# Performance work log

Hardware: AMD Instinct MI355X
Metric: run time of the kernel (lower is better)

Reference implementation:

```python
import jax, jax.numpy as jnp
import numpy as np

B, T, F, L, E, H, A, V = 64, 32, 512, 196, 512, 512, 512, 10000


def setup_inputs() -> dict:
    key = jax.random.key(0)
    ks = jax.random.split(key, 24)
    s = 0.02
    features = jax.random.normal(ks[0], (B, F, L), dtype=jnp.float32)
    captions = jax.random.randint(ks[1], (B, T), 0, V)
    lengths = jnp.sort(jax.random.randint(ks[2], (B,), 2, T + 1))[::-1]
    lengths = lengths.at[0].set(T)  # ensure max(decode_lengths) == T-1 (static)
    return {
        "features": features,
        "captions": captions,
        "lengths": lengths,
        "W_emb": jax.random.normal(ks[3], (V, E)) * s,
        "W_enc": jax.random.normal(ks[4], (A, F)) * s,
        "b_enc": jnp.zeros((A,)),
        "W_dec": jax.random.normal(ks[5], (A, H)) * s,
        "b_dec": jnp.zeros((A,)),
        "W_full": jax.random.normal(ks[6], (1, A)) * s,
        "b_full": jnp.zeros((1,)),
        "W_fbeta": jax.random.normal(ks[7], (F, H)) * s,
        "b_fbeta": jnp.zeros((F,)),
        "W_ih": jax.random.normal(ks[8], (4 * H, E + F)) * s,
        "W_hh": jax.random.normal(ks[9], (4 * H, H)) * s,
        "b_ih": jnp.zeros((4 * H,)),
        "b_hh": jnp.zeros((4 * H,)),
        "W_out": jax.random.normal(ks[10], (V, H)) * s,
        "b_out": jnp.zeros((V,)),
        "W_init_h": jax.random.normal(ks[11], (H, F)) * s,
        "b_init_h": jnp.zeros((H,)),
        "W_init_c": jax.random.normal(ks[12], (H, F)) * s,
        "b_init_c": jnp.zeros((H,)),
    }


def reference(features, captions, lengths, W_emb, W_enc, b_enc, W_dec, b_dec,
              W_full, b_full, W_fbeta, b_fbeta, W_ih, W_hh, b_ih, b_hh,
              W_out, b_out, W_init_h, b_init_h, W_init_c, b_init_c):
    Bv, Fv, Lv = features.shape
    Tmax = captions.shape[1] - 1  # max(decode_lengths), static (lengths[0]==T)
    feat_r = features.reshape(Bv, -1, Fv)          # [B, L, F] (torch .view semantics)
    en_att = feat_r @ W_enc.T + b_enc              # [B, L, A], step-invariant
    mean_f = features.mean(axis=2)                 # [B, F]
    h0 = mean_f @ W_init_h.T + b_init_h            # [B, H]
    c0 = mean_f @ W_init_c.T + b_init_c
    emb = W_emb[captions]                          # [B, T, E]
    dec_len = lengths - 1                          # [B]

    def step(carry, xs):
        h, c = carry
        emb_t, i = xs
        de = h @ W_dec.T + b_dec                                   # [B, A]
        full = (jnp.tanh(en_att + de[:, None, :]) @ W_full.T)[..., 0] + b_full[0]  # [B, L]
        alpha = jax.nn.softmax(full, axis=1)                       # [B, L]
        z = jnp.einsum('blf,bl->bf', feat_r, alpha)                # [B, F]
        z = z * jax.nn.sigmoid(h @ W_fbeta.T + b_fbeta)
        x = jnp.concatenate([emb_t, z], axis=1)                    # [B, E+F]
        gates = x @ W_ih.T + b_ih + h @ W_hh.T + b_hh              # [B, 4H]
        ig, fg, gg, og = jnp.split(gates, 4, axis=1)
        c_new = jax.nn.sigmoid(fg) * c + jax.nn.sigmoid(ig) * jnp.tanh(gg)
        h_new = jax.nn.sigmoid(og) * jnp.tanh(c_new)
        out = h_new @ W_out.T + b_out                              # [B, V] (dropout: eval)
        active = (dec_len > i)[:, None]                            # ragged mask
        h = jnp.where(active, h_new, h)
        c = jnp.where(active, c_new, c)
        pred = jnp.where(active, out, 0.0)
        alpha_m = jnp.where(active, alpha, 0.0)
        return (h, c), (pred, alpha_m)

    emb_steps = jnp.swapaxes(emb[:, :Tmax, :], 0, 1)               # [Tmax, B, E]
    (_, _), (preds, alphas) = jax.lax.scan(step, (h0, c0), (emb_steps, jnp.arange(Tmax)))
    predictions = jnp.swapaxes(preds, 0, 1)                        # [B, Tmax, V]
    alphas = jnp.swapaxes(alphas, 0, 1)                            # [B, Tmax, L]
    return predictions, alphas
```

## Files before the change

### kernel.cpp

```cpp
#include <hip/hip_runtime.h>


typedef unsigned short ushort_t;
typedef __attribute__((ext_vector_type(8))) short short8;
typedef __attribute__((ext_vector_type(4))) float f32x4;

__device__ __forceinline__ float bf2f(ushort_t u) {
    unsigned x = ((unsigned)u) << 16;
    float f;
    __builtin_memcpy(&f, &x, 4);
    return f;
}
__device__ __forceinline__ ushort_t f2bf(float f) {
    unsigned x;
    __builtin_memcpy(&x, &f, 4);
    unsigned r = (x + 0x7fffu + ((x >> 16) & 1u)) >> 16;
    return (ushort_t)r;
}
__device__ __forceinline__ float sigmoidf_(float x) { return 1.f / (1.f + __expf(-x)); }
__device__ __forceinline__ float tanh_fast(float x) {
    float e = __expf(2.f * x);
    return 1.f - 2.f / (e + 1.f);
}
__device__ __forceinline__ float wred_sum(float v) {
    #pragma unroll
    for (int m = 32; m; m >>= 1) v += __shfl_xor(v, m, 64);
    return v;
}
__device__ __forceinline__ float wred_max(float v) {
    #pragma unroll
    for (int m = 32; m; m >>= 1) v = fmaxf(v, __shfl_xor(v, m, 64));
    return v;
}

__device__ __forceinline__ float aload_f(const float* p) {
    return __hip_atomic_load((float*)p, __ATOMIC_RELAXED, __HIP_MEMORY_SCOPE_AGENT);
}
__device__ __forceinline__ void astore_f(float* p, float v) {
    __hip_atomic_store(p, v, __ATOMIC_RELAXED, __HIP_MEMORY_SCOPE_AGENT);
}
__device__ __forceinline__ unsigned aload_u(const unsigned* p) {
    return __hip_atomic_load((unsigned*)p, __ATOMIC_RELAXED, __HIP_MEMORY_SCOPE_AGENT);
}
__device__ __forceinline__ void astore_u(unsigned* p, unsigned v) {
    __hip_atomic_store(p, v, __ATOMIC_RELAXED, __HIP_MEMORY_SCOPE_AGENT);
}
__device__ __forceinline__ int aload_i(const int* p) {
    return __hip_atomic_load((int*)p, __ATOMIC_RELAXED, __HIP_MEMORY_SCOPE_AGENT);
}
__device__ __forceinline__ void astore_i(int* p, int v) {
    __hip_atomic_store(p, v, __ATOMIC_RELAXED, __HIP_MEMORY_SCOPE_AGENT);
}

#define KEXP2 2.8853901817779268f

__global__ void detect_kernel(const unsigned* __restrict__ feat_raw, int* __restrict__ flag,
                              int* __restrict__ flags) {
    int lane = threadIdx.x;
    #pragma unroll
    for (int i = 0; i < 16; ++i) flags[lane + i * 64] = 0;
    unsigned u = feat_raw[lane];
    unsigned e = (u >> 7) & 0xffu;
    bool bf_like = (e >= 105 && e <= 133);
    unsigned long long m = __ballot(bf_like);
    if (lane == 0) *flag = (__popcll(m) >= 40) ? 0 : 1;
}

#define NCVT 19
struct CvtArgs {
    const void* src[NCVT];
    void* dst[NCVT];
    int n[NCVT];
};

__global__ __launch_bounds__(256) void convert_kernel(CvtArgs a, const int* __restrict__ flag) {
    const int ai = blockIdx.y;
    const int n = a.n[ai];
    const int base = (blockIdx.x * 256 + threadIdx.x) * 8;
    if (base >= n) return;
    ushort_t* dst = (ushort_t*)a.dst[ai];
    if (*flag) {
        const float* s = (const float*)a.src[ai];
        #pragma unroll
        for (int i = 0; i < 8; ++i) {
            int idx = base + i;
            if (idx < n) dst[idx] = f2bf(s[idx]);
        }
    } else {
        const ushort_t* s = (const ushort_t*)a.src[ai];
        #pragma unroll
        for (int i = 0; i < 8; ++i) {
            int idx = base + i;
            if (idx < n) dst[idx] = s[idx];
        }
    }
}

__global__ __launch_bounds__(256) void embrows_kernel(const void* __restrict__ Wemb,
                                                      const int* __restrict__ captions,
                                                      const int* __restrict__ flag,
                                                      ushort_t* __restrict__ emb_c) {
    const int tb = blockIdx.x;
    const int t = tb >> 6, b = tb & 63;
    const int cap = captions[b * 32 + t];
    const int e0 = threadIdx.x;
    if (*flag) {
        const float* s = (const float*)Wemb + cap * 512;
        emb_c[tb * 512 + e0] = f2bf(s[e0]);
        emb_c[tb * 512 + e0 + 256] = f2bf(s[e0 + 256]);
    } else {
        const ushort_t* s = (const ushort_t*)Wemb + cap * 512;
        emb_c[tb * 512 + e0] = s[e0];
        emb_c[tb * 512 + e0 + 256] = s[e0 + 256];
    }
}

__global__ void prepw2_kernel(const ushort_t* __restrict__ wf, const ushort_t* __restrict__ bfc,
                              float* __restrict__ w2) {
    int tid = threadIdx.x;
    float w = bf2f(wf[tid]);
    w2[tid] = -2.f * w;
    float s = wred_sum(w);
    __shared__ float r8[8];
    if ((tid & 63) == 0) r8[tid >> 6] = s;
    __syncthreads();
    if (tid == 0) {
        float tot = r8[0] + r8[1] + r8[2] + r8[3] + r8[4] + r8[5] + r8[6] + r8[7];
        w2[512] = tot + bf2f(bfc[0]);
    }
}

template <class AROW, class BROW, class EPI>
__device__ __forceinline__ void gemm_tile(AROW arow, BROW brow, EPI epi) {
    __shared__ __align__(16) ushort_t As[64][40];
    __shared__ __align__(16) ushort_t Bs[64][40];
    const int tid = threadIdx.x;
    const int row = tid >> 2, ks = (tid & 3) << 3;
    const int wave = tid >> 6, lane = tid & 63;
    const int quad = lane >> 4, l15 = lane & 15;
    f32x4 acc[4];
    #pragma unroll
    for (int s = 0; s < 4; ++s) acc[s] = (f32x4){0.f, 0.f, 0.f, 0.f};
    const ushort_t* ap = arow(row);
    const ushort_t* bp = brow(row);
    for (int k0 = 0; k0 < 512; k0 += 32) {
        short8 av = {0, 0, 0, 0, 0, 0, 0, 0};
        short8 bv = {0, 0, 0, 0, 0, 0, 0, 0};
        if (ap) av = *(const short8*)(ap + k0 + ks);
        if (bp) bv = *(const short8*)(bp + k0 + ks);
        __syncthreads();
        *(short8*)&As[row][ks] = av;
        *(short8*)&Bs[row][ks] = bv;
        __syncthreads();
        short8 af = *(const short8*)&As[(wave << 4) + l15][quad << 3];
        #pragma unroll
        for (int s = 0; s < 4; ++s) {
            short8 bfr = *(const short8*)&Bs[(s << 4) + l15][quad << 3];
            acc[s] = __builtin_amdgcn_mfma_f32_16x16x32_bf16(af, bfr, acc[s], 0, 0, 0);
        }
    }
    epi((wave << 4) + (quad << 2), l15, acc);
}

__global__ __launch_bounds__(256) void mean_kernel(const ushort_t* __restrict__ features,
                                                   ushort_t* __restrict__ mean_bf) {
    const int b = blockIdx.x;
    const int wave = threadIdx.x >> 6, lane = threadIdx.x & 63;
    const ushort_t* fb = features + b * 512 * 196;
    for (int f = wave; f < 512; f += 4) {
        const ushort_t* r = fb + f * 196;
        float s = bf2f(r[lane]) + bf2f(r[lane + 64]) + bf2f(r[lane + 128]);
        if (lane < 4) s += bf2f(r[lane + 192]);
        s = wred_sum(s);
        if (lane == 0) mean_bf[b * 512 + f] = f2bf(s * (1.f / 196.f));
    }
}

__global__ __launch_bounds__(256) void init_kernel(
    const ushort_t* __restrict__ mean_bf, const ushort_t* __restrict__ Winh,
    const ushort_t* __restrict__ binh, const ushort_t* __restrict__ Winc,
    const ushort_t* __restrict__ binc, ushort_t* __restrict__ h_bf,
    float* __restrict__ cbuf) {
    const int n0 = blockIdx.x << 6;
    gemm_tile(
        [&](int r) { return mean_bf + r * 512; },
        [&](int r) {
            int n = n0 + r;
            return (n < 512) ? (Winh + n * 512) : (Winc + (n - 512) * 512);
        },
        [&](int mb, int l15, const f32x4* acc) {
            #pragma unroll
            for (int s = 0; s < 4; ++s) {
                int n = n0 + (s << 4) + l15;
                #pragma unroll
                for (int r = 0; r < 4; ++r) {
                    int b = mb + r;
                    if (n < 512)
                        h_bf[b * 512 + n] = f2bf(acc[s][r] + bf2f(binh[n]));
                    else
                        cbuf[b * 512 + (n - 512)] = acc[s][r] + bf2f(binc[n - 512]);
                }
            }
        });
}

__global__ __launch_bounds__(256) void enatt_kernel(const ushort_t* __restrict__ feat,
                                                    const ushort_t* __restrict__ Wenc,
                                                    const ushort_t* __restrict__ benc,
                                                    ushort_t* __restrict__ en_att) {
    const int m0 = blockIdx.y << 6, n0 = blockIdx.x << 6;
    gemm_tile(
        [&](int r) { return feat + (m0 + r) * 512; },
        [&](int r) { return Wenc + (n0 + r) * 512; },
        [&](int mb, int l15, const f32x4* acc) {
            #pragma unroll
            for (int s = 0; s < 4; ++s) {
                int n = n0 + (s << 4) + l15;
                float bias = bf2f(benc[n]);
                #pragma unroll
                for (int r = 0; r < 4; ++r) {
                    int m = m0 + mb + r;
                    en_att[m * 512 + n] = f2bf(acc[s][r] + bias);
                }
            }
        });
}

__global__ __launch_bounds__(256) void ec_kernel(const ushort_t* __restrict__ emb_c,
                                                 const ushort_t* __restrict__ Wih,
                                                 const ushort_t* __restrict__ bih,
                                                 const ushort_t* __restrict__ bhh,
                                                 float* __restrict__ ec) {
    const int t = blockIdx.y, n0 = blockIdx.x << 6;
    gemm_tile(
        [&](int r) { return emb_c + (t * 64 + r) * 512; },
        [&](int r) { return Wih + (n0 + r) * 1024; },
        [&](int mb, int l15, const f32x4* acc) {
            #pragma unroll
            for (int s = 0; s < 4; ++s) {
                int j = n0 + (s << 4) + l15;
                float bias = bf2f(bih[j]) + bf2f(bhh[j]);
                #pragma unroll
                for (int r = 0; r < 4; ++r) {
                    int b = mb + r;
                    ec[(t * 64 + b) * 2048 + j] = acc[s][r] + bias;
                }
            }
        });
}

struct LoopArgs {
    const ushort_t* W3c;
    const ushort_t* bdec;
    const ushort_t* bfb;
    const ushort_t* en_att;
    const ushort_t* feat;
    const ushort_t* Wih;
    const float* w2;
    const float* ec;
    const int* lengths;
    const int* flag;
    ushort_t* h_bf;
    ushort_t* z_bf;
    ushort_t* H_all;
    float* cbuf;
    float* deK;
    float* fgate;
    float* hh;
    float* fullv;
    void* out_base;
    int* flags;
};

__global__ __launch_bounds__(512, 2) void loop_kernel(LoopArgs A) {
    const int blk = blockIdx.x, tid = threadIdx.x;
    const int wave = tid >> 6, lane = tid & 63;
    const int quad = lane >> 4, l15 = lane & 15;
    const int g = blk >> 6, local = blk & 63;
    int* fbase = A.flags + g * 256;

    __shared__ __align__(16) ushort_t enS[49 * 512];
    __shared__ __align__(16) ushort_t ftS[196 * 128];
    __shared__ __align__(16) ushort_t AsL[16][520];
    __shared__ float smem[2048];
    __shared__ float fullS[200];
    __shared__ float red8[16];

    const int f32o = *A.flag;
    const int b0 = g << 4;
    const int Tg = A.lengths[b0] - 1;

    const bool roleA = local < 24;
    const int bB = b0 + (local >> 2);
    const int qB = local & 3;
    const int lenB = A.lengths[bB];
    const bool roleC = local < 32;
    const int dtC = local;

    unsigned* h_u32 = (unsigned*)A.h_bf;
    unsigned* z_u32 = (unsigned*)A.z_bf;

    float w2r[8];
    {
        f32x4 w0 = *(const f32x4*)(A.w2 + lane * 8);
        f32x4 w1 = *(const f32x4*)(A.w2 + lane * 8 + 4);
        w2r[0] = w0[0]; w2r[1] = w0[1]; w2r[2] = w0[2]; w2r[3] = w0[3];
        w2r[4] = w1[0]; w2r[5] = w1[1]; w2r[6] = w1[2]; w2r[7] = w1[3];
    }
    const float fullc = A.w2[512];

    {
        const short8* src = (const short8*)(A.en_att + ((size_t)bB * 196 + qB * 49) * 512);
        short8* dst = (short8*)enS;
        for (int i = tid; i < 49 * 64; i += 512) dst[i] = src[i];
        const ushort_t* fsrc = A.feat + (size_t)bB * 100352 + qB * 128;
        short8* fdst = (short8*)ftS;
        for (int i = tid; i < 196 * 16; i += 512) {
            int l = i >> 4, c = i & 15;
            fdst[i] = *(const short8*)(fsrc + l * 512 + c * 8);
        }
    }

    for (int t = 0; t < Tg; ++t) {
        if (roleA) {
            if (wave == 0 && t > 0) {
                const int* fp = fbase + (lane & 31);
                for (;;) {
                    if (__all(aload_i(fp) >= t)) break;
                    __builtin_amdgcn_s_sleep(1);
                }
                asm volatile("" ::: "memory");
            }
            __syncthreads();
            for (int i = tid; i < 4096; i += 512) {
                int r = i >> 8, c = i & 255;
                *(unsigned*)&AsL[r][c << 1] = aload_u(h_u32 + ((b0 + r) << 8) + c);
            }
            __syncthreads();
            const int nt = local * 8 + wave;
            const ushort_t* br = A.W3c + ((nt << 4) + l15) * 512 + (quad << 3);
            const ushort_t* arl = &AsL[l15][quad << 3];
            f32x4 acc = {0.f, 0.f, 0.f, 0.f};
            #pragma unroll
            for (int k0 = 0; k0 < 512; k0 += 32)
                acc = __builtin_amdgcn_mfma_f32_16x16x32_bf16(
                    *(const short8*)(arl + k0), *(const short8*)(br + k0), acc, 0, 0, 0);
            const int n = (nt << 4) + l15;
            #pragma unroll
            for (int r = 0; r < 4; ++r) {
                const int b = b0 + (quad << 2) + r;
                float v = acc[r];
                if (n < 512)
                    astore_f(A.deK + b * 512 + n, (v + bf2f(A.bdec[n])) * KEXP2);
                else if (n < 1024)
                    astore_f(A.fgate + b * 512 + (n - 512),
                             sigmoidf_(v + bf2f(A.bfb[n - 512])));
                else
                    astore_f(A.hh + b * 2048 + (n - 1024), v);
            }
            asm volatile("s_waitcnt vmcnt(0)" ::: "memory");
            __syncthreads();
            if (tid == 0) astore_i(fbase + 32 + local, t + 1);
        }

        {
            if (wave == 0) {
                const int* fp = fbase + 32 + (lane & 7);
                for (;;) {
                    if (__all(aload_i(fp) >= t + 1)) break;
                    __builtin_amdgcn_s_sleep(1);
                }
                asm volatile("" ::: "memory");
            }
            __syncthreads();
            const bool act = (lenB - 1) > t;
            const size_t aoff = 19840000ull + ((size_t)bB * 31 + t) * 196;
            if (act) {
                float dkr[8];
                const float* dk = A.deK + bB * 512 + lane * 8;
                #pragma unroll
                for (int j = 0; j < 8; ++j) dkr[j] = aload_f(dk + j);
                for (int i = wave; i < 49; i += 8) {
                    short8 ev = *(const short8*)(enS + i * 512 + lane * 8);
                    float acc = 0.f;
                    #pragma unroll
                    for (int j = 0; j < 8; ++j) {
                        float e2 = __builtin_amdgcn_exp2f(
                            fmaf(bf2f((ushort_t)ev[j]), KEXP2, dkr[j]));
                        acc = fmaf(w2r[j], __builtin_amdgcn_rcpf(e2 + 1.f), acc);
                    }
                    acc = wred_sum(acc);
                    if (lane == 0)
                        astore_f(A.fullv + bB * 196 + qB * 49 + i, acc + fullc);
                }
            }
            asm volatile("s_waitcnt vmcnt(0)" ::: "memory");
            __syncthreads();
            if (tid == 0) astore_i(fbase + 128 + local, t + 1);
            if (wave == 0) {
                const int* fp = fbase + 128 + (local & ~3) + (lane & 3);
                for (;;) {
                    if (__all(aload_i(fp) >= t + 1)) break;
                    __builtin_amdgcn_s_sleep(1);
                }
                asm volatile("" ::: "memory");
            }
            __syncthreads();
            if (act) {
                float v = (tid < 196) ? aload_f(A.fullv + bB * 196 + tid) : -1e30f;
                float wm = wred_max(v);
                if (lane == 0) red8[wave] = wm;
                __syncthreads();
                float mx = fmaxf(fmaxf(fmaxf(red8[0], red8[1]), fmaxf(red8[2], red8[3])),
                                 fmaxf(fmaxf(red8[4], red8[5]), fmaxf(red8[6], red8[7])));
                float e = (tid < 196) ? __expf(v - mx) : 0.f;
                float sw = wred_sum(e);
                if (lane == 0) red8[8 + wave] = sw;
                __syncthreads();
                float tot = red8[8] + red8[9] + red8[10] + red8[11] +
                            red8[12] + red8[13] + red8[14] + red8[15];
                float inv = 1.f / tot;
                float a = e * inv;
                if (tid < 196) {
                    fullS[tid] = a;
                    if (qB == 0) {
                        if (f32o) ((float*)A.out_base)[aoff + tid] = a;
                        else ((ushort_t*)A.out_base)[aoff + tid] = f2bf(a);
                    }
                }
                __syncthreads();
                const int fl = tid & 127, gq = tid >> 7;
                float zacc = 0.f;
                #pragma unroll 4
                for (int l = gq; l < 196; l += 4)
                    zacc = fmaf(fullS[l], bf2f(ftS[l * 128 + fl]), zacc);
                smem[256 + (gq << 7) + fl] = zacc;
                __syncthreads();
                if (tid < 64) {
                    const int f0l = tid << 1;
                    float z0 = smem[256 + f0l] + smem[384 + f0l] +
                               smem[512 + f0l] + smem[640 + f0l];
                    float z1 = smem[257 + f0l] + smem[385 + f0l] +
                               smem[513 + f0l] + smem[641 + f0l];
                    const int f0 = (qB << 7) + f0l;
                    z0 *= aload_f(A.fgate + bB * 512 + f0);
                    z1 *= aload_f(A.fgate + bB * 512 + f0 + 1);
                    unsigned zp = (unsigned)f2bf(z0) | ((unsigned)f2bf(z1) << 16);
                    astore_u(z_u32 + bB * 256 + (f0 >> 1), zp);
                }
            } else {
                if (qB == 0 && tid < 196) {
                    if (f32o) ((float*)A.out_base)[aoff + tid] = 0.f;
                    else ((ushort_t*)A.out_base)[aoff + tid] = 0;
                }
            }
            asm volatile("s_waitcnt vmcnt(0)" ::: "memory");
            __syncthreads();
            if (tid == 0) astore_i(fbase + 64 + local, t + 1);
        }

        if (roleC) {
            if (wave == 0) {
                const int* zp = fbase + 64 + lane;
                for (;;) {
                    int v1 = aload_i(zp);
                    int v2 = (lane < 4)
                                 ? aload_i(fbase + 32 + 8 + lane * 4 + (dtC >> 3))
                                 : 0x7fffffff;
                    if (__all(v1 >= t + 1 && v2 >= t + 1)) break;
                    __builtin_amdgcn_s_sleep(1);
                }
                asm volatile("" ::: "memory");
            }
            __syncthreads();
            float pe[8], ph[8];
            #pragma unroll
            for (int k = 0; k < 8; ++k) { pe[k] = 0.f; ph[k] = 0.f; }
            if (tid < 128) {
                const int bl = tid >> 3, p = tid & 7;
                const int bE = b0 + bl;
                const int dimE = (dtC << 4) + (p << 1);
                const int eb = (t * 64 + bE) * 2048, hb = bE * 2048;
                pe[0] = A.ec[eb + dimE];         pe[1] = A.ec[eb + dimE + 1];
                pe[2] = A.ec[eb + 512 + dimE];   pe[3] = A.ec[eb + 512 + dimE + 1];
                pe[4] = A.ec[eb + 1024 + dimE];  pe[5] = A.ec[eb + 1024 + dimE + 1];
                pe[6] = A.ec[eb + 1536 + dimE];  pe[7] = A.ec[eb + 1536 + dimE + 1];
                ph[0] = aload_f(A.hh + hb + dimE);
                ph[1] = aload_f(A.hh + hb + dimE + 1);
                ph[2] = aload_f(A.hh + hb + 512 + dimE);
                ph[3] = aload_f(A.hh + hb + 512 + dimE + 1);
                ph[4] = aload_f(A.hh + hb + 1024 + dimE);
                ph[5] = aload_f(A.hh + hb + 1024 + dimE + 1);
                ph[6] = aload_f(A.hh + hb + 1536 + dimE);
                ph[7] = aload_f(A.hh + hb + 1536 + dimE + 1);
            }
            for (int i = tid; i < 4096; i += 512) {
                int r = i >> 8, c = i & 255;
                *(unsigned*)&AsL[r][c << 1] = aload_u(z_u32 + ((b0 + r) << 8) + c);
            }
            __syncthreads();
            const int gw = wave & 3, kh = wave >> 2;
            const int j = (gw << 9) + (dtC << 4) + l15;
            const ushort_t* br = A.Wih + j * 1024 + 512 + (kh << 8) + (quad << 3);
            const ushort_t* arl = &AsL[l15][(kh << 8) + (quad << 3)];
            f32x4 acc = {0.f, 0.f, 0.f, 0.f};
            #pragma unroll
            for (int k0 = 0; k0 < 256; k0 += 32)
                acc = __builtin_amdgcn_mfma_f32_16x16x32_bf16(
                    *(const short8*)(arl + k0), *(const short8*)(br + k0), acc, 0, 0, 0);
            #pragma unroll
            for (int r = 0; r < 4; ++r)
                smem[(wave << 8) + (((quad << 2) + r) << 4) + l15] = acc[r];
            __syncthreads();
            if (tid < 128) {
                const int bl = tid >> 3, p = tid & 7;
                const int b = b0 + bl;
                const int i0 = (bl << 4) + (p << 1);
                const int dim = (dtC << 4) + (p << 1);
                float ig0 = smem[i0] + smem[1024 + i0] + pe[0] + ph[0];
                float ig1 = smem[i0 + 1] + smem[1025 + i0] + pe[1] + ph[1];
                float fg0 = smem[256 + i0] + smem[1280 + i0] + pe[2] + ph[2];
                float fg1 = smem[257 + i0] + smem[1281 + i0] + pe[3] + ph[3];
                float gg0 = smem[512 + i0] + smem[1536 + i0] + pe[4] + ph[4];
                float gg1 = smem[513 + i0] + smem[1537 + i0] + pe[5] + ph[5];
                float og0 = smem[768 + i0] + smem[1792 + i0] + pe[6] + ph[6];
                float og1 = smem[769 + i0] + smem[1793 + i0] + pe[7] + ph[7];
                float co0 = A.cbuf[b * 512 + dim];
                float co1 = A.cbuf[b * 512 + dim + 1];
                float cn0 = sigmoidf_(fg0) * co0 + sigmoidf_(ig0) * tanh_fast(gg0);
                float hn0 = sigmoidf_(og0) * tanh_fast(cn0);
                float cn1 = sigmoidf_(fg1) * co1 + sigmoidf_(ig1) * tanh_fast(gg1);
                float hn1 = sigmoidf_(og1) * tanh_fast(cn1);
                unsigned hp = (unsigned)f2bf(hn0) | ((unsigned)f2bf(hn1) << 16);
                *(unsigned*)&A.H_all[(t * 64 + b) * 512 + dim] = hp;
                if (A.lengths[b] - 1 > t) {
                    A.cbuf[b * 512 + dim] = cn0;
                    A.cbuf[b * 512 + dim + 1] = cn1;
                    astore_u(h_u32 + b * 256 + (dim >> 1), hp);
                }
            }
            asm volatile("s_waitcnt vmcnt(0)" ::: "memory");
            __syncthreads();
            if (tid == 0) astore_i(fbase + dtC, t + 1);
        }
    }

    if (qB == 0) {
        for (int t = Tg; t < 31; ++t) {
            if (tid < 196) {
                const size_t aoff = 19840000ull + ((size_t)bB * 31 + t) * 196;
                if (f32o) ((float*)A.out_base)[aoff + tid] = 0.f;
                else ((ushort_t*)A.out_base)[aoff + tid] = 0;
            }
        }
    }
}

__global__ __launch_bounds__(256) void preds_kernel(
    const ushort_t* __restrict__ H_all, const ushort_t* __restrict__ Wout,
    const ushort_t* __restrict__ bout, const int* __restrict__ lengths,
    const int* __restrict__ flag, void* __restrict__ out_base) {
    const int t = blockIdx.x, n0 = blockIdx.y << 6;
    const int f32o = *flag;
    gemm_tile(
        [&](int r) { return H_all + (t * 64 + r) * 512; },
        [&](int r) -> const ushort_t* {
            int n = n0 + r;
            return (n < 10000) ? (Wout + n * 512) : (const ushort_t*)nullptr;
        },
        [&](int mb, int l15, const f32x4* acc) {
            #pragma unroll
            for (int s = 0; s < 4; ++s) {
                int n = n0 + (s << 4) + l15;
                if (n >= 10000) continue;
                float bias = bf2f(bout[n]);
                #pragma unroll
                for (int r = 0; r < 4; ++r) {
                    int b = mb + r;
                    bool act = lengths[b] > t + 1;
                    float val = act ? (acc[s][r] + bias) : 0.f;
                    size_t off = (size_t)b * 310000 + t * 10000 + n;
                    if (f32o) ((float*)out_base)[off] = val;
                    else ((ushort_t*)out_base)[off] = act ? f2bf(val) : (ushort_t)0;
                }
            }
        });
}

extern "C" void kernel_launch(void* const* d_in, const int* in_sizes, int n_in,
                              void* d_out, int out_size, void* d_ws, size_t ws_size,
                              hipStream_t stream) {
    const void* features = d_in[0];
    const int* captions = (const int*)d_in[1];
    const int* lengths = (const int*)d_in[2];
    const void* W_emb = d_in[3];

    char* ws = (char*)d_ws;
    size_t o = 0;
    auto alloc = [&](size_t bytes) {
        size_t r = o;
        o += (bytes + 255) & ~(size_t)255;
        return r;
    };
    ushort_t* feat_c  = (ushort_t*)(ws + alloc(6422528ull * 2));
    ushort_t* Wenc_c  = (ushort_t*)(ws + alloc(262144ull * 2));
    ushort_t* benc_c  = (ushort_t*)(ws + alloc(512 * 2));
    ushort_t* W3c     = (ushort_t*)(ws + alloc(3072ull * 512 * 2));
    ushort_t* bdec_c  = (ushort_t*)(ws + alloc(512 * 2));
    ushort_t* wfull_c = (ushort_t*)(ws + alloc(512 * 2));
    ushort_t* bfull_c = (ushort_t*)(ws + alloc(2));
    ushort_t* bfb_c   = (ushort_t*)(ws + alloc(512 * 2));
    ushort_t* Wih_c   = (ushort_t*)(ws + alloc(2097152ull * 2));
    ushort_t* bih_c   = (ushort_t*)(ws + alloc(2048 * 2));
    ushort_t* bhh_c   = (ushort_t*)(ws + alloc(2048 * 2));
    ushort_t* Wout_c  = (ushort_t*)(ws + alloc(5120000ull * 2));
    ushort_t* bout_c  = (ushort_t*)(ws + alloc(10000 * 2));
    ushort_t* Winh_c  = (ushort_t*)(ws + alloc(262144ull * 2));
    ushort_t* binh_c  = (ushort_t*)(ws + alloc(512 * 2));
    ushort_t* Winc_c  = (ushort_t*)(ws + alloc(262144ull * 2));
    ushort_t* binc_c  = (ushort_t*)(ws + alloc(512 * 2));
    ushort_t* emb_c   = (ushort_t*)(ws + alloc(1984ull * 512 * 2));
    ushort_t* en_att  = (ushort_t*)(ws + alloc(12544ull * 512 * 2));
    float*    ec      = (float*)(ws + alloc(1984ull * 2048 * 4));
    ushort_t* H_all   = (ushort_t*)(ws + alloc(1984ull * 512 * 2));
    ushort_t* h_bf    = (ushort_t*)(ws + alloc(64 * 512 * 2));
    float*    cbuf    = (float*)(ws + alloc(64 * 512 * 4));
    float*    deK     = (float*)(ws + alloc(64 * 512 * 4));
    float*    fgate   = (float*)(ws + alloc(64 * 512 * 4));
    float*    hh      = (float*)(ws + alloc(64ull * 2048 * 4));
    ushort_t* z_bf    = (ushort_t*)(ws + alloc(64 * 512 * 2));
    ushort_t* mean_bf = (ushort_t*)(ws + alloc(64 * 512 * 2));
    float*    fullv   = (float*)(ws + alloc(64 * 196 * 4));
    float*    w2buf   = (float*)(ws + alloc(513 * 4));
    int*      flag    = (int*)(ws + alloc(256));
    int*      flags   = (int*)(ws + alloc(1024 * 4));

    detect_kernel<<<1, 64, 0, stream>>>((const unsigned*)features, flag, flags);

    CvtArgs ca;
    const void* srcs[NCVT] = {features, d_in[4], d_in[5], d_in[6], d_in[7], d_in[8],
                              d_in[9], d_in[10], d_in[11], d_in[12], d_in[13], d_in[14],
                              d_in[15], d_in[16], d_in[17], d_in[18], d_in[19], d_in[20],
                              d_in[21]};
    void* dsts[NCVT] = {feat_c, Wenc_c, benc_c, W3c , bdec_c, wfull_c, bfull_c,
                        W3c + 262144 , bfb_c, Wih_c, W3c + 524288 ,
                        bih_c, bhh_c, Wout_c, bout_c, Winh_c, binh_c, Winc_c, binc_c};
    int ns[NCVT] = {6422528, 262144, 512, 262144, 512, 512, 1, 262144, 512,
                    2097152, 1048576, 2048, 2048, 5120000, 10000, 262144, 512,
                    262144, 512};
    for (int i = 0; i < NCVT; ++i) {
        ca.src[i] = srcs[i];
        ca.dst[i] = dsts[i];
        ca.n[i] = ns[i];
    }
    convert_kernel<<<dim3(3136, NCVT), 256, 0, stream>>>(ca, flag);
    embrows_kernel<<<1984, 256, 0, stream>>>(W_emb, captions, flag, emb_c);
    prepw2_kernel<<<1, 512, 0, stream>>>(wfull_c, bfull_c, w2buf);

    mean_kernel<<<64, 256, 0, stream>>>(feat_c, mean_bf);
    init_kernel<<<16, 256, 0, stream>>>(mean_bf, Winh_c, binh_c, Winc_c, binc_c,
                                        h_bf, cbuf);
    enatt_kernel<<<dim3(8, 196), 256, 0, stream>>>(feat_c, Wenc_c, benc_c, en_att);
    ec_kernel<<<dim3(32, 31), 256, 0, stream>>>(emb_c, Wih_c, bih_c, bhh_c, ec);

    LoopArgs la;
    la.W3c = W3c; la.bdec = bdec_c; la.bfb = bfb_c;
    la.en_att = en_att; la.feat = feat_c; la.Wih = Wih_c;
    la.w2 = w2buf; la.ec = ec; la.lengths = lengths; la.flag = flag;
    la.h_bf = h_bf; la.z_bf = z_bf; la.H_all = H_all;
    la.cbuf = cbuf; la.deK = deK; la.fgate = fgate; la.hh = hh;
    la.fullv = fullv; la.out_base = d_out; la.flags = flags;
    loop_kernel<<<256, 512, 0, stream>>>(la);

    preds_kernel<<<dim3(31, 157), 256, 0, stream>>>(H_all, Wout_c, bout_c, lengths,
                                                    flag, d_out);
}
```

Baseline: 1.177 ms.

## Remove separate h-projection phase from recurrent loop, fold into per-block compute

The dedicated phase where 24 blocks computed the decoder-attention, f-beta gate and W_hh projections for all batches, followed by a grid-wide flag wait, is removed. Each attention block now computes its own batch's decoder projection (using a pre-transposed W_dec) and its quarter of the f-beta gate with scalar FMAs. The W_hh term moves into the LSTM gate MFMA alongside the z term, and h is double-buffered so the next step's reads do not race with writes. This drops one inter-block synchronisation stage per timestep, at the cost of redundant dec-projection work across the 4 blocks per batch. It also adds spin caps to the flag waits and flattens the convert grid so no blocks are launched past each array's end.

```diff
diff --git a/kernel.cpp b/kernel.cpp
--- a/kernel.cpp
+++ b/kernel.cpp
@@ -4,6 +4,8 @@
 typedef unsigned short ushort_t;
 typedef __attribute__((ext_vector_type(8))) short short8;
 typedef __attribute__((ext_vector_type(4))) float f32x4;
+
+#define SPIN_CAP (1 << 22)
 
 __device__ __forceinline__ float bf2f(ushort_t u) {
     unsigned x = ((unsigned)u) << 16;
@@ -71,12 +73,14 @@
     const void* src[NCVT];
     void* dst[NCVT];
     int n[NCVT];
+    int cub[NCVT + 1];
 };
 
 __global__ __launch_bounds__(256) void convert_kernel(CvtArgs a, const int* __restrict__ flag) {
-    const int ai = blockIdx.y;
+    int bx = blockIdx.x, ai = 0;
+    while (bx >= a.cub[ai + 1]) ++ai;
     const int n = a.n[ai];
-    const int base = (blockIdx.x * 256 + threadIdx.x) * 8;
+    const int base = (bx - a.cub[ai]) * 2048 + threadIdx.x * 8;
     if (base >= n) return;
     ushort_t* dst = (ushort_t*)a.dst[ai];
     if (*flag) {
@@ -93,6 +97,22 @@
             int idx = base + i;
             if (idx < n) dst[idx] = s[idx];
         }
+    }
+}
+
+__global__ __launch_bounds__(256) void transpose_wdec_kernel(const ushort_t* __restrict__ W3c,
+                                                             ushort_t* __restrict__ WdT) {
+    __shared__ ushort_t tile[64][65];
+    const int ta = (blockIdx.x & 7) << 6;
+    const int tk = (blockIdx.x >> 3) << 6;
+    for (int i = threadIdx.x; i < 4096; i += 256) {
+        int r = i >> 6, c = i & 63;
+        tile[r][c] = W3c[(ta + r) * 512 + tk + c];
+    }
+    __syncthreads();
+    for (int i = threadIdx.x; i < 4096; i += 256) {
+        int r = i >> 6, c = i & 63;
+        WdT[(tk + r) * 512 + ta + c] = tile[c][r];
     }
 }
 
@@ -251,6 +271,7 @@
 
 struct LoopArgs {
     const ushort_t* W3c;
+    const ushort_t* WdT;
     const ushort_t* bdec;
     const ushort_t* bfb;
     const ushort_t* en_att;
@@ -264,9 +285,6 @@
     ushort_t* z_bf;
     ushort_t* H_all;
     float* cbuf;
-    float* deK;
-    float* fgate;
-    float* hh;
     float* fullv;
     void* out_base;
     int* flags;
@@ -281,8 +299,11 @@
 
     __shared__ __align__(16) ushort_t enS[49 * 512];
     __shared__ __align__(16) ushort_t ftS[196 * 128];
-    __shared__ __align__(16) ushort_t AsL[16][520];
-    __shared__ float smem[2048];
+    __shared__ __align__(16) ushort_t AsL[32][520];
+    __shared__ float smem[4096];
+    __shared__ float hS[512];
+    __shared__ float deS[512];
+    __shared__ float fgS[128];
     __shared__ float fullS[200];
     __shared__ float red8[16];
 
@@ -290,7 +311,6 @@
     const int b0 = g << 4;
     const int Tg = A.lengths[b0] - 1;
 
-    const bool roleA = local < 24;
     const int bB = b0 + (local >> 2);
     const int qB = local & 3;
     const int lenB = A.lengths[bB];
@@ -320,66 +340,62 @@
             fdst[i] = *(const short8*)(fsrc + l * 512 + c * 8);
         }
     }
+    __syncthreads();
 
     for (int t = 0; t < Tg; ++t) {
-        if (roleA) {
+        const bool act = (lenB - 1) > t;
+        const size_t aoff = 19840000ull + ((size_t)bB * 31 + t) * 196;
+
+        if (act) {
             if (wave == 0 && t > 0) {
                 const int* fp = fbase + (lane & 31);
+                int spins = 0;
                 for (;;) {
                     if (__all(aload_i(fp) >= t)) break;
+                    if (++spins > SPIN_CAP) break;
                     __builtin_amdgcn_s_sleep(1);
                 }
                 asm volatile("" ::: "memory");
             }
             __syncthreads();
-            for (int i = tid; i < 4096; i += 512) {
-                int r = i >> 8, c = i & 255;
-                *(unsigned*)&AsL[r][c << 1] = aload_u(h_u32 + ((b0 + r) << 8) + c);
-            }
-            __syncthreads();
-            const int nt = local * 8 + wave;
-            const ushort_t* br = A.W3c + ((nt << 4) + l15) * 512 + (quad << 3);
-            const ushort_t* arl = &AsL[l15][quad << 3];
-            f32x4 acc = {0.f, 0.f, 0.f, 0.f};
-            #pragma unroll
-            for (int k0 = 0; k0 < 512; k0 += 32)
-                acc = __builtin_amdgcn_mfma_f32_16x16x32_bf16(
-                    *(const short8*)(arl + k0), *(const short8*)(br + k0), acc, 0, 0, 0);
-            const int n = (nt << 4) + l15;
-            #pragma unroll
-            for (int r = 0; r < 4; ++r) {
-                const int b = b0 + (quad << 2) + r;
-                float v = acc[r];
-                if (n < 512)
-                    astore_f(A.deK + b * 512 + n, (v + bf2f(A.bdec[n])) * KEXP2);
-                else if (n < 1024)
-                    astore_f(A.fgate + b * 512 + (n - 512),
-                             sigmoidf_(v + bf2f(A.bfb[n - 512])));
-                else
-                    astore_f(A.hh + b * 2048 + (n - 1024), v);
-            }
-            asm volatile("s_waitcnt vmcnt(0)" ::: "memory");
-            __syncthreads();
-            if (tid == 0) astore_i(fbase + 32 + local, t + 1);
-        }
-
-        {
-            if (wave == 0) {
-                const int* fp = fbase + 32 + (lane & 7);
-                for (;;) {
-                    if (__all(aload_i(fp) >= t + 1)) break;
-                    __builtin_amdgcn_s_sleep(1);
-                }
-                asm volatile("" ::: "memory");
-            }
-            __syncthreads();
-            const bool act = (lenB - 1) > t;
-            const size_t aoff = 19840000ull + ((size_t)bB * 31 + t) * 196;
-            if (act) {
+            {
+                const unsigned* hsrc = h_u32 + ((t & 1) << 14) + bB * 256;
+                if (tid < 256) {
+                    unsigned v = aload_u(hsrc + tid);
+                    hS[tid * 2] = bf2f((ushort_t)(v & 0xffffu));
+                    hS[tid * 2 + 1] = bf2f((ushort_t)(v >> 16));
+                }
+            }
+            __syncthreads();
+            {
+                float p[8];
+                #pragma unroll
+                for (int j = 0; j < 8; ++j) p[j] = 0.f;
+                const ushort_t* wt = A.WdT + (wave << 6) * 512 + (lane << 3);
+                #pragma unroll 4
+                for (int i = 0; i < 64; ++i) {
+                    short8 wv = *(const short8*)(wt + i * 512);
+                    float hk = hS[(wave << 6) + i];
+                    #pragma unroll
+                    for (int j = 0; j < 8; ++j)
+                        p[j] = fmaf(bf2f((ushort_t)wv[j]), hk, p[j]);
+                }
+                #pragma unroll
+                for (int j = 0; j < 8; ++j)
+                    smem[(wave << 9) + (lane << 3) + j] = p[j];
+            }
+            __syncthreads();
+            {
+                float dsum = 0.f;
+                #pragma unroll
+                for (int q = 0; q < 8; ++q) dsum += smem[(q << 9) + tid];
+                deS[tid] = (dsum + bf2f(A.bdec[tid])) * KEXP2;
+            }
+            __syncthreads();
+            {
                 float dkr[8];
-                const float* dk = A.deK + bB * 512 + lane * 8;
                 #pragma unroll
-                for (int j = 0; j < 8; ++j) dkr[j] = aload_f(dk + j);
+                for (int j = 0; j < 8; ++j) dkr[j] = deS[lane * 8 + j];
                 for (int i = wave; i < 49; i += 8) {
                     short8 ev = *(const short8*)(enS + i * 512 + lane * 8);
                     float acc = 0.f;
@@ -394,163 +410,188 @@
                         astore_f(A.fullv + bB * 196 + qB * 49 + i, acc + fullc);
                 }
             }
-            asm volatile("s_waitcnt vmcnt(0)" ::: "memory");
-            __syncthreads();
-            if (tid == 0) astore_i(fbase + 128 + local, t + 1);
+        }
+        asm volatile("s_waitcnt vmcnt(0)" ::: "memory");
+        __syncthreads();
+        if (tid == 0) astore_i(fbase + 128 + local, t + 1);
+
+        if (act) {
+            {
+                const int fl_ = tid >> 2, kq_ = tid & 3;
+                const ushort_t* wr = A.W3c + (512 + (qB << 7) + fl_) * 512 + (kq_ << 7);
+                float a2 = 0.f;
+                #pragma unroll 4
+                for (int k = 0; k < 128; k += 8) {
+                    short8 wv = *(const short8*)(wr + k);
+                    #pragma unroll
+                    for (int j = 0; j < 8; ++j)
+                        a2 = fmaf(bf2f((ushort_t)wv[j]), hS[(kq_ << 7) + k + j], a2);
+                }
+                smem[tid] = a2;
+            }
             if (wave == 0) {
                 const int* fp = fbase + 128 + (local & ~3) + (lane & 3);
+                int spins = 0;
                 for (;;) {
                     if (__all(aload_i(fp) >= t + 1)) break;
+                    if (++spins > SPIN_CAP) break;
                     __builtin_amdgcn_s_sleep(1);
                 }
                 asm volatile("" ::: "memory");
             }
             __syncthreads();
+            if (tid < 128)
+                fgS[tid] = sigmoidf_(smem[tid << 2] + smem[(tid << 2) | 1] +
+                                     smem[(tid << 2) | 2] + smem[(tid << 2) | 3] +
+                                     bf2f(A.bfb[(qB << 7) + tid]));
+            float v = (tid < 196) ? aload_f(A.fullv + bB * 196 + tid) : -1e30f;
+            float wm = wred_max(v);
+            if (lane == 0) red8[wave] = wm;
+            __syncthreads();
+            float mx = fmaxf(fmaxf(fmaxf(red8[0], red8[1]), fmaxf(red8[2], red8[3])),
+                             fmaxf(fmaxf(red8[4], red8[5]), fmaxf(red8[6], red8[7])));
+            float e = (tid < 196) ? __expf(v - mx) : 0.f;
+            float sw = wred_sum(e);
+            if (lane == 0) red8[8 + wave] = sw;
+            __syncthreads();
+            float tot = red8[8] + red8[9] + red8[10] + red8[11] +
+                        red8[12] + red8[13] + red8[14] + red8[15];
+            float inv = 1.f / tot;
+            float a = e * inv;
+            if (tid < 196) fullS[tid] = a;
+            __syncthreads();
+            const int fl = tid & 127, gq = tid >> 7;
+            float zacc = 0.f;
+            #pragma unroll 4
+            for (int l = gq; l < 196; l += 4)
+                zacc = fmaf(fullS[l], bf2f(ftS[l * 128 + fl]), zacc);
+            smem[256 + (gq << 7) + fl] = zacc;
+            __syncthreads();
+            if (tid < 64) {
+                const int f0l = tid << 1;
+                float z0 = smem[256 + f0l] + smem[384 + f0l] +
+                           smem[512 + f0l] + smem[640 + f0l];
+                float z1 = smem[257 + f0l] + smem[385 + f0l] +
+                           smem[513 + f0l] + smem[641 + f0l];
+                z0 *= fgS[f0l];
+                z1 *= fgS[f0l + 1];
+                unsigned zp = (unsigned)f2bf(z0) | ((unsigned)f2bf(z1) << 16);
+                astore_u(z_u32 + bB * 256 + (qB << 6) + tid, zp);
+            }
+        }
+        asm volatile("s_waitcnt vmcnt(0)" ::: "memory");
+        __syncthreads();
+        if (tid == 0) astore_i(fbase + 64 + local, t + 1);
+        if (qB == 0 && tid < 196) {
             if (act) {
-                float v = (tid < 196) ? aload_f(A.fullv + bB * 196 + tid) : -1e30f;
-                float wm = wred_max(v);
-                if (lane == 0) red8[wave] = wm;
-                __syncthreads();
-                float mx = fmaxf(fmaxf(fmaxf(red8[0], red8[1]), fmaxf(red8[2], red8[3])),
-                                 fmaxf(fmaxf(red8[4], red8[5]), fmaxf(red8[6], red8[7])));
-                float e = (tid < 196) ? __expf(v - mx) : 0.f;
-                float sw = wred_sum(e);
-                if (lane == 0) red8[8 + wave] = sw;
-                __syncthreads();
-                float tot = red8[8] + red8[9] + red8[10] + red8[11] +
-                            red8[12] + red8[13] + red8[14] + red8[15];
-                float inv = 1.f / tot;
-                float a = e * inv;
-                if (tid < 196) {
-                    fullS[tid] = a;
-                    if (qB == 0) {
-                        if (f32o) ((float*)A.out_base)[aoff + tid] = a;
-                        else ((ushort_t*)A.out_base)[aoff + tid] = f2bf(a);
-                    }
-                }
-                __syncthreads();
-                const int fl = tid & 127, gq = tid >> 7;
-                float zacc = 0.f;
-                #pragma unroll 4
-                for (int l = gq; l < 196; l += 4)
-                    zacc = fmaf(fullS[l], bf2f(ftS[l * 128 + fl]), zacc);
-                smem[256 + (gq << 7) + fl] = zacc;
-                __syncthreads();
-                if (tid < 64) {
-                    const int f0l = tid << 1;
-                    float z0 = smem[256 + f0l] + smem[384 + f0l] +
-                               smem[512 + f0l] + smem[640 + f0l];
-                    float z1 = smem[257 + f0l] + smem[385 + f0l] +
-                               smem[513 + f0l] + smem[641 + f0l];
-                    const int f0 = (qB << 7) + f0l;
-                    z0 *= aload_f(A.fgate + bB * 512 + f0);
-                    z1 *= aload_f(A.fgate + bB * 512 + f0 + 1);
-                    unsigned zp = (unsigned)f2bf(z0) | ((unsigned)f2bf(z1) << 16);
-                    astore_u(z_u32 + bB * 256 + (f0 >> 1), zp);
-                }
+                if (f32o) ((float*)A.out_base)[aoff + tid] = fullS[tid];
+                else ((ushort_t*)A.out_base)[aoff + tid] = f2bf(fullS[tid]);
             } else {
-                if (qB == 0 && tid < 196) {
-                    if (f32o) ((float*)A.out_base)[aoff + tid] = 0.f;
-                    else ((ushort_t*)A.out_base)[aoff + tid] = 0;
-                }
-            }
-            asm volatile("s_waitcnt vmcnt(0)" ::: "memory");
-            __syncthreads();
-            if (tid == 0) astore_i(fbase + 64 + local, t + 1);
+                if (f32o) ((float*)A.out_base)[aoff + tid] = 0.f;
+                else ((ushort_t*)A.out_base)[aoff + tid] = 0;
+            }
         }
 
         if (roleC) {
             if (wave == 0) {
                 const int* zp = fbase + 64 + lane;
+                int spins = 0;
                 for (;;) {
-                    int v1 = aload_i(zp);
-                    int v2 = (lane < 4)
-                                 ? aload_i(fbase + 32 + 8 + lane * 4 + (dtC >> 3))
-                                 : 0x7fffffff;
-                    if (__all(v1 >= t + 1 && v2 >= t + 1)) break;
+                    if (__all(aload_i(zp) >= t + 1)) break;
+                    if (++spins > SPIN_CAP) break;
                     __builtin_amdgcn_s_sleep(1);
                 }
                 asm volatile("" ::: "memory");
             }
             __syncthreads();
-            float pe[8], ph[8];
+            float pe[8];
             #pragma unroll
-            for (int k = 0; k < 8; ++k) { pe[k] = 0.f; ph[k] = 0.f; }
+            for (int k = 0; k < 8; ++k) pe[k] = 0.f;
             if (tid < 128) {
                 const int bl = tid >> 3, p = tid & 7;
                 const int bE = b0 + bl;
                 const int dimE = (dtC << 4) + (p << 1);
-                const int eb = (t * 64 + bE) * 2048, hb = bE * 2048;
+                const int eb = (t * 64 + bE) * 2048;
                 pe[0] = A.ec[eb + dimE];         pe[1] = A.ec[eb + dimE + 1];
                 pe[2] = A.ec[eb + 512 + dimE];   pe[3] = A.ec[eb + 512 + dimE + 1];
                 pe[4] = A.ec[eb + 1024 + dimE];  pe[5] = A.ec[eb + 1024 + dimE + 1];
                 pe[6] = A.ec[eb + 1536 + dimE];  pe[7] = A.ec[eb + 1536 + dimE + 1];
-                ph[0] = aload_f(A.hh + hb + dimE);
-                ph[1] = aload_f(A.hh + hb + dimE + 1);
-                ph[2] = aload_f(A.hh + hb + 512 + dimE);
-                ph[3] = aload_f(A.hh + hb + 512 + dimE + 1);
-                ph[4] = aload_f(A.hh + hb + 1024 + dimE);
-                ph[5] = aload_f(A.hh + hb + 1024 + dimE + 1);
-                ph[6] = aload_f(A.hh + hb + 1536 + dimE);
-                ph[7] = aload_f(A.hh + hb + 1536 + dimE + 1);
-            }
-            for (int i = tid; i < 4096; i += 512) {
-                int r = i >> 8, c = i & 255;
-                *(unsigned*)&AsL[r][c << 1] = aload_u(z_u32 + ((b0 + r) << 8) + c);
+            }
+            {
+                const unsigned* hsrc = h_u32 + ((t & 1) << 14);
+                for (int i = tid; i < 4096; i += 512) {
+                    int r = i >> 8, c = i & 255;
+                    *(unsigned*)&AsL[r][c << 1] = aload_u(z_u32 + ((b0 + r) << 8) + c);
+                    *(unsigned*)&AsL[16 + r][c << 1] = aload_u(hsrc + ((b0 + r) << 8) + c);
+                }
             }
             __syncthreads();
             const int gw = wave & 3, kh = wave >> 2;
             const int j = (gw << 9) + (dtC << 4) + l15;
-            const ushort_t* br = A.Wih + j * 1024 + 512 + (kh << 8) + (quad << 3);
-            const ushort_t* arl = &AsL[l15][(kh << 8) + (quad << 3)];
+            const ushort_t* brz = A.Wih + j * 1024 + 512 + (kh << 8) + (quad << 3);
+            const ushort_t* brh = A.W3c + (1024 + j) * 512 + (kh << 8) + (quad << 3);
+            const ushort_t* arz = &AsL[l15][(kh << 8) + (quad << 3)];
+            const ushort_t* arh = &AsL[16 + l15][(kh << 8) + (quad << 3)];
             f32x4 acc = {0.f, 0.f, 0.f, 0.f};
             #pragma unroll
-            for (int k0 = 0; k0 < 256; k0 += 32)
+            for (int k0 = 0; k0 < 256; k0 += 32) {
                 acc = __builtin_amdgcn_mfma_f32_16x16x32_bf16(
-                    *(const short8*)(arl + k0), *(const short8*)(br + k0), acc, 0, 0, 0);
+                    *(const short8*)(arz + k0), *(const short8*)(brz + k0), acc, 0, 0, 0);
+                acc = __builtin_amdgcn_mfma_f32_16x16x32_bf16(
+                    *(const short8*)(arh + k0), *(const short8*)(brh + k0), acc, 0, 0, 0);
+            }
             #pragma unroll
             for (int r = 0; r < 4; ++r)
                 smem[(wave << 8) + (((quad << 2) + r) << 4) + l15] = acc[r];
             __syncthreads();
+            float cn0 = 0.f, cn1 = 0.f;
+            unsigned hpw = 0;
+            bool activeB = false;
+            int bQ = 0, dimQ = 0;
             if (tid < 128) {
                 const int bl = tid >> 3, p = tid & 7;
-                const int b = b0 + bl;
+                bQ = b0 + bl;
+                dimQ = (dtC << 4) + (p << 1);
                 const int i0 = (bl << 4) + (p << 1);
-                const int dim = (dtC << 4) + (p << 1);
-                float ig0 = smem[i0] + smem[1024 + i0] + pe[0] + ph[0];
-                float ig1 = smem[i0 + 1] + smem[1025 + i0] + pe[1] + ph[1];
-                float fg0 = smem[256 + i0] + smem[1280 + i0] + pe[2] + ph[2];
-                float fg1 = smem[257 + i0] + smem[1281 + i0] + pe[3] + ph[3];
-                float gg0 = smem[512 + i0] + smem[1536 + i0] + pe[4] + ph[4];
-                float gg1 = smem[513 + i0] + smem[1537 + i0] + pe[5] + ph[5];
-                float og0 = smem[768 + i0] + smem[1792 + i0] + pe[6] + ph[6];
-                float og1 = smem[769 + i0] + smem[1793 + i0] + pe[7] + ph[7];
-                float co0 = A.cbuf[b * 512 + dim];
-                float co1 = A.cbuf[b * 512 + dim + 1];
-                float cn0 = sigmoidf_(fg0) * co0 + sigmoidf_(ig0) * tanh_fast(gg0);
+                float ig0 = smem[i0] + smem[1024 + i0] + pe[0];
+                float ig1 = smem[i0 + 1] + smem[1025 + i0] + pe[1];
+                float fg0 = smem[256 + i0] + smem[1280 + i0] + pe[2];
+                float fg1 = smem[257 + i0] + smem[1281 + i0] + pe[3];
+                float gg0 = smem[512 + i0] + smem[1536 + i0] + pe[4];
+                float gg1 = smem[513 + i0] + smem[1537 + i0] + pe[5];
+                float og0 = smem[768 + i0] + smem[1792 + i0] + pe[6];
+                float og1 = smem[769 + i0] + smem[1793 + i0] + pe[7];
+                float co0 = A.cbuf[bQ * 512 + dimQ];
+                float co1 = A.cbuf[bQ * 512 + dimQ + 1];
+                cn0 = sigmoidf_(fg0) * co0 + sigmoidf_(ig0) * tanh_fast(gg0);
                 float hn0 = sigmoidf_(og0) * tanh_fast(cn0);
-                float cn1 = sigmoidf_(fg1) * co1 + sigmoidf_(ig1) * tanh_fast(gg1);
+                cn1 = sigmoidf_(fg1) * co1 + sigmoidf_(ig1) * tanh_fast(gg1);
                 float hn1 = sigmoidf_(og1) * tanh_fast(cn1);
-                unsigned hp = (unsigned)f2bf(hn0) | ((unsigned)f2bf(hn1) << 16);
-                *(unsigned*)&A.H_all[(t * 64 + b) * 512 + dim] = hp;
-                if (A.lengths[b] - 1 > t) {
-                    A.cbuf[b * 512 + dim] = cn0;
-                    A.cbuf[b * 512 + dim + 1] = cn1;
-                    astore_u(h_u32 + b * 256 + (dim >> 1), hp);
-                }
+                activeB = (A.lengths[bQ] - 1) > t;
+                unsigned newp = (unsigned)f2bf(hn0) | ((unsigned)f2bf(hn1) << 16);
+                unsigned oldp = *(const unsigned*)&AsL[16 + bl][dimQ];
+                hpw = activeB ? newp : oldp;
+                astore_u(h_u32 + (((t + 1) & 1) << 14) + bQ * 256 + (dimQ >> 1), hpw);
             }
             asm volatile("s_waitcnt vmcnt(0)" ::: "memory");
             __syncthreads();
             if (tid == 0) astore_i(fbase + dtC, t + 1);
+            if (tid < 128) {
+                *(unsigned*)&A.H_all[(t * 64 + bQ) * 512 + dimQ] = hpw;
+                if (activeB) {
+                    A.cbuf[bQ * 512 + dimQ] = cn0;
+                    A.cbuf[bQ * 512 + dimQ + 1] = cn1;
+                }
+            }
         }
     }
 
     if (qB == 0) {
         for (int t = Tg; t < 31; ++t) {
             if (tid < 196) {
-                const size_t aoff = 19840000ull + ((size_t)bB * 31 + t) * 196;
-                if (f32o) ((float*)A.out_base)[aoff + tid] = 0.f;
-                else ((ushort_t*)A.out_base)[aoff + tid] = 0;
+                const size_t aoff2 = 19840000ull + ((size_t)bB * 31 + t) * 196;
+                if (f32o) ((float*)A.out_base)[aoff2 + tid] = 0.f;
+                else ((ushort_t*)A.out_base)[aoff2 + tid] = 0;
             }
         }
     }
@@ -606,6 +647,7 @@
     ushort_t* Wenc_c  = (ushort_t*)(ws + alloc(262144ull * 2));
     ushort_t* benc_c  = (ushort_t*)(ws + alloc(512 * 2));
     ushort_t* W3c     = (ushort_t*)(ws + alloc(3072ull * 512 * 2));
+    ushort_t* WdT     = (ushort_t*)(ws + alloc(262144ull * 2));
     ushort_t* bdec_c  = (ushort_t*)(ws + alloc(512 * 2));
     ushort_t* wfull_c = (ushort_t*)(ws + alloc(512 * 2));
     ushort_t* bfull_c = (ushort_t*)(ws + alloc(2));
@@ -623,11 +665,8 @@
     ushort_t* en_att  = (ushort_t*)(ws + alloc(12544ull * 512 * 2));
     float*    ec      = (float*)(ws + alloc(1984ull * 2048 * 4));
     ushort_t* H_all   = (ushort_t*)(ws + alloc(1984ull * 512 * 2));
-    ushort_t* h_bf    = (ushort_t*)(ws + alloc(64 * 512 * 2));
+    ushort_t* h_bf    = (ushort_t*)(ws + alloc(2ull * 64 * 512 * 2));
     float*    cbuf    = (float*)(ws + alloc(64 * 512 * 4));
-    float*    deK     = (float*)(ws + alloc(64 * 512 * 4));
-    float*    fgate   = (float*)(ws + alloc(64 * 512 * 4));
-    float*    hh      = (float*)(ws + alloc(64ull * 2048 * 4));
     ushort_t* z_bf    = (ushort_t*)(ws + alloc(64 * 512 * 2));
     ushort_t* mean_bf = (ushort_t*)(ws + alloc(64 * 512 * 2));
     float*    fullv   = (float*)(ws + alloc(64 * 196 * 4));
@@ -648,12 +687,15 @@
     int ns[NCVT] = {6422528, 262144, 512, 262144, 512, 512, 1, 262144, 512,
                     2097152, 1048576, 2048, 2048, 5120000, 10000, 262144, 512,
                     262144, 512};
+    ca.cub[0] = 0;
     for (int i = 0; i < NCVT; ++i) {
         ca.src[i] = srcs[i];
         ca.dst[i] = dsts[i];
         ca.n[i] = ns[i];
-    }
-    convert_kernel<<<dim3(3136, NCVT), 256, 0, stream>>>(ca, flag);
+        ca.cub[i + 1] = ca.cub[i] + (ns[i] + 2047) / 2048;
+    }
+    convert_kernel<<<ca.cub[NCVT], 256, 0, stream>>>(ca, flag);
+    transpose_wdec_kernel<<<64, 256, 0, stream>>>(W3c, WdT);
     embrows_kernel<<<1984, 256, 0, stream>>>(W_emb, captions, flag, emb_c);
     prepw2_kernel<<<1, 512, 0, stream>>>(wfull_c, bfull_c, w2buf);
 
@@ -664,12 +706,12 @@
     ec_kernel<<<dim3(32, 31), 256, 0, stream>>>(emb_c, Wih_c, bih_c, bhh_c, ec);
 
     LoopArgs la;
-    la.W3c = W3c; la.bdec = bdec_c; la.bfb = bfb_c;
+    la.W3c = W3c; la.WdT = WdT; la.bdec = bdec_c; la.bfb = bfb_c;
     la.en_att = en_att; la.feat = feat_c; la.Wih = Wih_c;
     la.w2 = w2buf; la.ec = ec; la.lengths = lengths; la.flag = flag;
     la.h_bf = h_bf; la.z_bf = z_bf; la.H_all = H_all;
-    la.cbuf = cbuf; la.deK = deK; la.fgate = fgate; la.hh = hh;
-    la.fullv = fullv; la.out_base = d_out; la.flags = flags;
+    la.cbuf = cbuf; la.fullv = fullv;
+    la.out_base = d_out; la.flags = flags;
     loop_kernel<<<256, 512, 0, stream>>>(la);
 
     preds_kernel<<<dim3(31, 157), 256, 0, stream>>>(H_all, Wout_c, bout_c, lengths,
```

After: 1.191 ms. About the same (+1.2%).
